# Kernel optimization log

Hardware: AMD Instinct MI355X
Metric: run time of the kernel (lower is better)

Reference implementation:

```python
import jax, jax.numpy as jnp
import numpy as np

B, S, D, H, KD, FF = 512, 128, 128, 8, 128, 512  # molecules, max atoms, embed, heads, key_dim(=embed), ffn
NEG = -1e9
EPS = 1e-3  # keras LayerNormalization default epsilon


def _layernorm(x, g, b):
    m = jnp.mean(x, axis=-1, keepdims=True)
    v = jnp.var(x, axis=-1, keepdims=True)
    return (x - m) * jax.lax.rsqrt(v + EPS) * g + b


def setup_inputs() -> dict:
    key = jax.random.key(0)
    k = jax.random.split(key, 8)
    # ragged molecule sizes in [32, 128]; deterministic so shapes are reproducible
    counts = 32 + ((np.arange(B) * 37) % 97)
    N = int(counts.sum())  # 40914
    mol = jnp.asarray(np.repeat(np.arange(B), counts), jnp.int32)  # sorted molecule ids
    picked = jnp.asarray((np.arange(B) * 13) % counts, jnp.int64)  # valid in-molecule atom index
    s = 0.05
    return {
        "atom_features": jax.random.normal(k[0], (N, D), jnp.float32),
        "Wq": jax.random.normal(k[1], (D, H, KD), jnp.float32) * s,
        "bq": jnp.zeros((H, KD), jnp.float32),
        "Wk": jax.random.normal(k[2], (D, H, KD), jnp.float32) * s,
        "bk": jnp.zeros((H, KD), jnp.float32),
        "Wv": jax.random.normal(k[3], (D, H, KD), jnp.float32) * s,
        "bv": jnp.zeros((H, KD), jnp.float32),
        "Wo": jax.random.normal(k[4], (H, KD, D), jnp.float32) * s,
        "bo": jnp.zeros((D,), jnp.float32),
        "W1": jax.random.normal(k[5], (D, FF), jnp.float32) * s,
        "b1": jnp.zeros((FF,), jnp.float32),
        "W2": jax.random.normal(k[6], (FF, D), jnp.float32) * s,
        "b2": jnp.zeros((D,), jnp.float32),
        "g1": jnp.ones((D,), jnp.float32),
        "beta1": jnp.zeros((D,), jnp.float32),
        "g2": jnp.ones((D,), jnp.float32),
        "beta2": jnp.zeros((D,), jnp.float32),
        "molecule_indicator": mol,
        "picked_atoms": picked,
    }


def _forward(atom_features, Wq, bq, Wk, bk, Wv, bv, Wo, bo, W1, b1, W2, b2,
             g1, beta1, g2, beta2, mol, picked):
    N = mol.shape[0]
    # --- PartitionPadding: pack ragged atoms -> [B, S, D] (every molecule nonempty,
    # so the zero-row filter keeps all B molecules in order) ---
    counts = jax.ops.segment_sum(jnp.ones((N,), jnp.int32), mol, num_segments=B)
    offsets = jnp.concatenate([jnp.zeros((1,), jnp.int32), jnp.cumsum(counts)[:-1]])
    pos = jnp.arange(N, dtype=jnp.int32) - offsets[mol]  # index within molecule
    x = jnp.zeros((B, S, D), atom_features.dtype).at[mol, pos].set(atom_features)
    mask = jnp.arange(S)[None, :] < counts[:, None]  # key padding mask [B, S]

    # --- masked MHA (keras MultiHeadAttention, key_dim = embed_dim) ---
    q = jnp.einsum('bsd,dhk->bshk', x, Wq) + bq
    kk = jnp.einsum('bsd,dhk->bshk', x, Wk) + bk
    v = jnp.einsum('bsd,dhk->bshk', x, Wv) + bv
    scores = jnp.einsum('bqhk,bshk->bhqs', q, kk) / jnp.sqrt(jnp.float32(KD))
    scores = jnp.where(mask[:, None, None, :], scores, NEG)
    attn = jax.nn.softmax(scores, axis=-1)
    ctx = jnp.einsum('bhqs,bshk->bqhk', attn, v)
    attn_out = jnp.einsum('bqhk,hkd->bqd', ctx, Wo) + bo

    # --- residual + LN + FFN + LN ---
    h = _layernorm(x + attn_out, g1, beta1)
    ffn = jax.nn.relu(h @ W1 + b1) @ W2 + b2
    out = _layernorm(h + ffn, g2, beta2)

    # --- gather_nd readout: one picked atom per molecule ---
    return out[jnp.arange(B), picked]  # [B, D]


def reference(atom_features, Wq, bq, Wk, bk, Wv, bv, Wo, bo, W1, b1, W2, b2,
              g1, beta1, g2, beta2, molecule_indicator, picked_atoms):
    return _forward(atom_features, Wq, bq, Wk, bk, Wv, bv, Wo, bo, W1, b1, W2, b2,
                    g1, beta1, g2, beta2, molecule_indicator, picked_atoms)
```

## Files before the change

kernel.cpp:

```cpp
#include <hip/hip_runtime.h>
#include <hip/hip_bf16.h>
#include <hip/hip_fp16.h>


#define BMOL 512

typedef _Float16 v2h __attribute__((ext_vector_type(2)));

#if defined(__has_builtin)
#if __has_builtin(__builtin_amdgcn_fdot2)
#define HAVE_FDOT2 1
#endif
#endif
static __device__ __forceinline__ float fdot2f(v2h a, v2h b, float c) {
#ifdef HAVE_FDOT2
    return __builtin_amdgcn_fdot2(a, b, c, false);
#else
    return c + (float)a[0] * (float)b[0] + (float)a[1] * (float)b[1];
#endif
}

__global__ __launch_bounds__(256) void k_front(
    const float* __restrict__ Wq, const float* __restrict__ bq,
    const float* __restrict__ Wk, const float* __restrict__ Wv,
    const float* __restrict__ Wo, const float* __restrict__ bv,
    const float* __restrict__ W1, const float* __restrict__ W2,
    const int* __restrict__ mol, int N, int noff,
    int* __restrict__ offs, __half* __restrict__ WVOp,
    __half* __restrict__ WQKp, float* __restrict__ bqk,
    float* __restrict__ bvoP, __half* __restrict__ W1p, __half* __restrict__ W2p)
{
    __shared__ float lds[2176];
    int bid = blockIdx.x, t = threadIdx.x;

    if (bid < 256) {
        bool qk = bid >= 128;
        int rel = bid & 127;
        int h = rel >> 4, tile = rel & 15;
        int dt = tile >> 2, ct = tile & 3;
        float* Avs = lds;
        float* Bos = lds + 1056;
        int ry = t >> 5, cx = t & 31;
        float acc[4] = {0.f, 0.f, 0.f, 0.f};
        const float* Asrc = qk ? Wq : Wv;
        for (int kk = 0; kk < 4; ++kk) {
            int r = t >> 3, e0 = (t & 7) * 4;
            float4 va = *(const float4*)(Asrc + (size_t)(dt * 32 + r) * 1024 + h * 128 + kk * 32 + e0);
            Avs[r * 33 + e0] = va.x; Avs[r * 33 + e0 + 1] = va.y;
            Avs[r * 33 + e0 + 2] = va.z; Avs[r * 33 + e0 + 3] = va.w;
            if (qk) {
                float4 vb = *(const float4*)(Wk + (size_t)(ct * 32 + r) * 1024 + h * 128 + kk * 32 + e0);
                Bos[(e0 + 0) * 33 + r] = vb.x;
                Bos[(e0 + 1) * 33 + r] = vb.y;
                Bos[(e0 + 2) * 33 + r] = vb.z;
                Bos[(e0 + 3) * 33 + r] = vb.w;
            } else {
                float4 vb = *(const float4*)(Wo + (size_t)h * 16384 + (size_t)(kk * 32 + r) * 128 + ct * 32 + e0);
                Bos[r * 33 + e0] = vb.x; Bos[r * 33 + e0 + 1] = vb.y;
                Bos[r * 33 + e0 + 2] = vb.z; Bos[r * 33 + e0 + 3] = vb.w;
            }
            __syncthreads();
            #pragma unroll
            for (int k = 0; k < 32; ++k) {
                float b = Bos[k * 33 + cx];
                #pragma unroll
                for (int i = 0; i < 4; ++i) acc[i] += Avs[(ry * 4 + i) * 33 + k] * b;
            }
            __syncthreads();
        }
        __half2 p0 = __floats2half2_rn(acc[0], acc[1]);
        __half2 p1 = __floats2half2_rn(acc[2], acc[3]);
        __half* dst = (qk ? WQKp : WVOp)
                    + (size_t)(h * 16 + dt * 4 + (ry >> 1)) * 1024
                    + (ct * 32 + cx) * 8 + (ry & 1) * 4;
        ((__half2*)dst)[0] = p0; ((__half2*)dst)[1] = p1;
        return;
    }
    bid -= 256;
    if (bid < 32) {
        int g = bid * 256 + t;
        int kg = g >> 9, f = g & 511;
        __half2 p[4];
        #pragma unroll
        for (int j = 0; j < 4; ++j) {
            float a = W1[(size_t)(kg * 8 + 2 * j) * 512 + f];
            float b = W1[(size_t)(kg * 8 + 2 * j + 1) * 512 + f];
            p[j] = __floats2half2_rn(a, b);
        }
        *(float4*)(W1p + (size_t)kg * 4096 + f * 8) = *(float4*)p;
        return;
    }
    bid -= 32;
    if (bid < 32) {
        int g = bid * 256 + t;
        int fg = g >> 7, c = g & 127;
        __half2 p[4];
        #pragma unroll
        for (int j = 0; j < 4; ++j) {
            float a = W2[(size_t)(fg * 8 + 2 * j) * 128 + c];
            float b = W2[(size_t)(fg * 8 + 2 * j + 1) * 128 + c];
            p[j] = __floats2half2_rn(a, b);
        }
        *(float4*)(W2p + (size_t)fg * 1024 + c * 8) = *(float4*)p;
        return;
    }
    bid -= 32;
    if (bid < 8) {
        int half = t >> 7, c = t & 127;
        float acc = 0.f;
        #pragma unroll 4
        for (int kk = 0; kk < 64; ++kk) {
            int k = bid * 128 + half * 64 + kk;
            acc += bv[k] * Wo[(size_t)k * 128 + c];
        }
        lds[half * 128 + c] = acc;
        __syncthreads();
        if (t < 128) bvoP[bid * 128 + t] = lds[t] + lds[128 + t];
        return;
    }
    bid -= 8;
    if (bid < 8) {
        int h = bid;
        if (t < 128) {
            const float* wk = Wk + (size_t)t * 1024 + h * 128;
            const float* bqh = bq + h * 128;
            float acc = 0.f;
            #pragma unroll 4
            for (int kd = 0; kd < 128; ++kd) acc += bqh[kd] * wk[kd];
            bqk[h * 128 + t] = acc;
        }
        return;
    }
    bid -= 8;
    {
        int i = bid * 256 + t;
        if (i < N) {
            if (i == 0) { offs[0] = 0; offs[BMOL] = N; }
            else if (mol[i] != mol[i - 1]) offs[mol[i]] = i;
        }
    }
}

__global__ __launch_bounds__(512) void k_attn_tail(
    const float* __restrict__ AF, const int* __restrict__ offs,
    const int* __restrict__ picked,
    const __half* __restrict__ WQKp, const float* __restrict__ bqk,
    const __half* __restrict__ WVOp, const float* __restrict__ bvoP,
    const float* __restrict__ bo,
    const float* __restrict__ g1, const float* __restrict__ be1,
    const __half* __restrict__ W1p, const float* __restrict__ b1,
    const __half* __restrict__ W2p, const float* __restrict__ b2,
    const float* __restrict__ g2, const float* __restrict__ be2,
    float* __restrict__ out)
{
    int b = blockIdx.x, t = threadIdx.x;
    int o0 = offs[b], cnt = offs[b + 1] - o0;
    __shared__ __half xs[128][136];
    __shared__ __half qsh[8][136];
    __shared__ float s[8 * 136];
    __shared__ float mh[8], lh[8];
    __shared__ float ws[2][1024];
    __shared__ __half wsh[1024];
    __shared__ float part[4][128];
    __shared__ float xp[128];
    __shared__ __half xph[128];
    __shared__ float h1raw[128], h1n[128];
    __shared__ __half h1nh[128];
    __shared__ __half msh[512];
    const float scale = 0.08838834764831843f;

    const float4* af4 = (const float4*)(AF + (size_t)o0 * 128);
    for (int p = t; p < cnt * 32; p += 512) {
        int i = p >> 5, d4 = p & 31;
        float4 v = af4[p];
        float2 st;
        ((__half2*)&st)[0] = __floats2half2_rn(v.x, v.y);
        ((__half2*)&st)[1] = __floats2half2_rn(v.z, v.w);
        *(float2*)(&xs[i][d4 * 4]) = st;
    }
    if (t < 128) {
        float v = AF[(size_t)(o0 + picked[b]) * 128 + t];
        xp[t] = v; xph[t] = (__half)v;
    }
    __syncthreads();
    {
        int h = t >> 6, d0 = (t & 63) * 2;
        const __half* wp = WQKp + ((size_t)(h * 16) * 128 + d0) * 8;
        const v2h* xh = (const v2h*)xph;
        float a0 = 0.f, a1 = 0.f;
        #pragma unroll 4
        for (int kg = 0; kg < 16; ++kg) {
            float4 r0 = *(const float4*)(wp + (size_t)kg * 1024);
            float4 r1 = *(const float4*)(wp + (size_t)kg * 1024 + 8);
            const v2h* h0 = (const v2h*)&r0;
            const v2h* h1 = (const v2h*)&r1;
            #pragma unroll
            for (int j = 0; j < 4; ++j) {
                v2h xv = xh[kg * 4 + j];
                a0 = fdot2f(xv, h0[j], a0);
                a1 = fdot2f(xv, h1[j], a1);
            }
        }
        qsh[h][d0]     = (__half)((a0 + bqk[h * 128 + d0]) * scale);
        qsh[h][d0 + 1] = (__half)((a1 + bqk[h * 128 + d0 + 1]) * scale);
    }
    __syncthreads();
    for (int p = t; p < cnt * 8; p += 512) {
        int i = p >> 3, h = p & 7;
        const float4* xr = (const float4*)xs[i];
        const float4* qr = (const float4*)qsh[h];
        float acc = 0.f;
        #pragma unroll 8
        for (int dq = 0; dq < 16; ++dq) {
            float4 xraw = xr[dq], qraw = qr[dq];
            const v2h* xh2 = (const v2h*)&xraw;
            const v2h* qh2 = (const v2h*)&qraw;
            acc = fdot2f(xh2[0], qh2[0], acc);
            acc = fdot2f(xh2[1], qh2[1], acc);
            acc = fdot2f(xh2[2], qh2[2], acc);
            acc = fdot2f(xh2[3], qh2[3], acc);
        }
        s[h * 136 + i] = acc;
    }
    __syncthreads();
    {
        int h = t >> 6, lane = t & 63;
        float m = -1e30f;
        for (int i = lane; i < cnt; i += 64) m = fmaxf(m, s[h * 136 + i]);
        #pragma unroll
        for (int off = 32; off; off >>= 1) m = fmaxf(m, __shfl_xor(m, off));
        float l = 0.f;
        for (int i = lane; i < cnt; i += 64) l += __expf(s[h * 136 + i] - m);
        #pragma unroll
        for (int off = 32; off; off >>= 1) l += __shfl_xor(l, off);
        if (lane == 0) { mh[h] = m; lh[h] = 1.f / l; }
    }
    __syncthreads();
    for (int p = t; p < cnt * 8; p += 512) {
        int i = p >> 3, h = p & 7;
        s[h * 136 + i] = __expf(s[h * 136 + i] - mh[h]) * lh[h];
    }
    __syncthreads();
    {
        int ih = t >> 8, hw = (t >> 5) & 7, qq = t & 31;
        float4 a4 = {0.f, 0.f, 0.f, 0.f};
        for (int i = ih; i < cnt; i += 2) {
            float sv = s[hw * 136 + i];
            float2 xraw = *(const float2*)(&xs[i][qq * 4]);
            const __half2* xh = (const __half2*)&xraw;
            float2 x0 = __half22float2(xh[0]), x1 = __half22float2(xh[1]);
            a4.x += sv * x0.x; a4.y += sv * x0.y; a4.z += sv * x1.x; a4.w += sv * x1.y;
        }
        *(float4*)(&ws[ih][hw * 128 + qq * 4]) = a4;
    }
    __syncthreads();
    {
        int k0 = t * 2;
        float v0 = ws[0][k0] + ws[1][k0];
        float v1 = ws[0][k0 + 1] + ws[1][k0 + 1];
        *(__half2*)(&wsh[k0]) = __floats2half2_rn(v0, v1);
    }
    __syncthreads();
    int wv = t >> 6, lane = t & 63;
    int kq = wv & 3, ch = wv >> 2;
    int c = ch * 64 + lane;
    {
        const __half* wp = WVOp + ((size_t)(kq * 32) * 128 + c) * 8;
        const v2h* wk = (const v2h*)wsh + kq * 128;
        float acc = 0.f;
        #pragma unroll 8
        for (int g = 0; g < 32; ++g) {
            float4 raw = *(const float4*)(wp + (size_t)g * 1024);
            const v2h* hp = (const v2h*)&raw;
            acc = fdot2f(hp[0], wk[g * 4 + 0], acc);
            acc = fdot2f(hp[1], wk[g * 4 + 1], acc);
            acc = fdot2f(hp[2], wk[g * 4 + 2], acc);
            acc = fdot2f(hp[3], wk[g * 4 + 3], acc);
        }
        part[kq][c] = acc;
    }
    __syncthreads();
    if (t < 128) {
        float acc = part[0][t] + part[1][t] + part[2][t] + part[3][t];
        float bias = bo[t];
        #pragma unroll
        for (int j = 0; j < 8; ++j) bias += bvoP[j * 128 + t];
        h1raw[t] = acc + bias + xp[t];
    }
    __syncthreads();
    {
        int l = t & 63;
        float a = h1raw[l], bb = h1raw[l + 64];
        float sm = a + bb, sq = a * a + bb * bb;
        #pragma unroll
        for (int off = 32; off; off >>= 1) { sm += __shfl_xor(sm, off); sq += __shfl_xor(sq, off); }
        float m = sm * (1.f / 128.f), var = sq * (1.f / 128.f) - m * m;
        float rs = rsqrtf(var + 1e-3f);
        if (t < 128) {
            float v = (h1raw[t] - m) * rs * g1[t] + be1[t];
            h1n[t] = v; h1nh[t] = (__half)v;
        }
    }
    __syncthreads();
    {
        const __half* wp = W1p + t * 8;
        const v2h* hk = (const v2h*)h1nh;
        float acc = 0.f;
        #pragma unroll 8
        for (int kg = 0; kg < 16; ++kg) {
            float4 raw = *(const float4*)(wp + (size_t)kg * 4096);
            const v2h* hp = (const v2h*)&raw;
            acc = fdot2f(hp[0], hk[kg * 4 + 0], acc);
            acc = fdot2f(hp[1], hk[kg * 4 + 1], acc);
            acc = fdot2f(hp[2], hk[kg * 4 + 2], acc);
            acc = fdot2f(hp[3], hk[kg * 4 + 3], acc);
        }
        msh[t] = (__half)fmaxf(acc + b1[t], 0.f);
    }
    __syncthreads();
    {
        const __half* wp = W2p + ((size_t)(kq * 16) * 128 + c) * 8;
        const v2h* mk = (const v2h*)msh + kq * 64;
        float acc = 0.f;
        #pragma unroll 8
        for (int g = 0; g < 16; ++g) {
            float4 raw = *(const float4*)(wp + (size_t)g * 1024);
            const v2h* hp = (const v2h*)&raw;
            acc = fdot2f(hp[0], mk[g * 4 + 0], acc);
            acc = fdot2f(hp[1], mk[g * 4 + 1], acc);
            acc = fdot2f(hp[2], mk[g * 4 + 2], acc);
            acc = fdot2f(hp[3], mk[g * 4 + 3], acc);
        }
        part[kq][c] = acc;
    }
    __syncthreads();
    if (t < 128) {
        float acc = part[0][t] + part[1][t] + part[2][t] + part[3][t];
        h1raw[t] = acc + b2[t] + h1n[t];
    }
    __syncthreads();
    {
        int l = t & 63;
        float a = h1raw[l], bb = h1raw[l + 64];
        float sm = a + bb, sq = a * a + bb * bb;
        #pragma unroll
        for (int off = 32; off; off >>= 1) { sm += __shfl_xor(sm, off); sq += __shfl_xor(sq, off); }
        float m = sm * (1.f / 128.f), var = sq * (1.f / 128.f) - m * m;
        float rs = rsqrtf(var + 1e-3f);
        if (t < 128) out[(size_t)b * 128 + t] = (h1raw[t] - m) * rs * g2[t] + be2[t];
    }
}

extern "C" void kernel_launch(void* const* d_in, const int* in_sizes, int n_in,
                              void* d_out, int out_size, void* d_ws, size_t ws_size,
                              hipStream_t stream) {
    const float* AF  = (const float*)d_in[0];
    const float* Wq  = (const float*)d_in[1];
    const float* bq  = (const float*)d_in[2];
    const float* Wk  = (const float*)d_in[3];
    const float* Wv  = (const float*)d_in[5];
    const float* bv  = (const float*)d_in[6];
    const float* Wo  = (const float*)d_in[7];
    const float* bo  = (const float*)d_in[8];
    const float* W1  = (const float*)d_in[9];
    const float* b1  = (const float*)d_in[10];
    const float* W2  = (const float*)d_in[11];
    const float* b2  = (const float*)d_in[12];
    const float* g1  = (const float*)d_in[13];
    const float* be1 = (const float*)d_in[14];
    const float* g2  = (const float*)d_in[15];
    const float* be2 = (const float*)d_in[16];
    const int* mol    = (const int*)d_in[17];
    const int* picked = (const int*)d_in[18];
    int N = in_sizes[0] / 128;
    int noff = (N + 255) / 256;

    char* ws = (char*)d_ws;
    int*    offs = (int*)ws;
    __half* WVOp = (__half*)(ws + 4096);
    __half* WQKp = (__half*)(ws + 266240);
    float*  bqk  = (float*)(ws + 528384);
    float*  bvoP = (float*)(ws + 532480);
    __half* W1p  = (__half*)(ws + 536576);
    __half* W2p  = (__half*)(ws + 667648);

    k_front<<<336 + noff, 256, 0, stream>>>(Wq, bq, Wk, Wv, Wo, bv, W1, W2,
                                            mol, N, noff,
                                            offs, WVOp, WQKp, bqk, bvoP, W1p, W2p);
    k_attn_tail<<<BMOL, 512, 0, stream>>>(AF, offs, picked, WQKp, bqk,
                                          WVOp, bvoP, bo, g1, be1, W1p, b1,
                                          W2p, b2, g2, be2, (float*)d_out);
}
```

Before: 36.05 us.

## Precompute per-molecule query projections in front kernel and batch tail over molecules

Query projection through Wq and Wk for each picked atom now runs in the front kernel: it binary-searches molecule offsets, loads picked rows and computes scaled query-key vectors per head, so the precomputed WQK product and bqk bias are no longer needed. The attention kernel only reads these vectors and writes the attention-weighted sums to workspace. A new tail kernel processes four molecules per block for Wo/V projection, layer norms and FFN, so each weight load is reused across four rows. This adds a third launch and a global round trip for intermediates, and puts more fp32 work in the front kernel.

```diff
diff --git a/kernel.cpp b/kernel.cpp
--- a/kernel.cpp
+++ b/kernel.cpp
@@ -21,44 +21,106 @@
 }
 
 __global__ __launch_bounds__(256) void k_front(
-    const float* __restrict__ Wq, const float* __restrict__ bq,
-    const float* __restrict__ Wk, const float* __restrict__ Wv,
-    const float* __restrict__ Wo, const float* __restrict__ bv,
-    const float* __restrict__ W1, const float* __restrict__ W2,
-    const int* __restrict__ mol, int N, int noff,
-    int* __restrict__ offs, __half* __restrict__ WVOp,
-    __half* __restrict__ WQKp, float* __restrict__ bqk,
-    float* __restrict__ bvoP, __half* __restrict__ W1p, __half* __restrict__ W2p)
+    const float* __restrict__ AF, const float* __restrict__ Wq,
+    const float* __restrict__ bq, const float* __restrict__ Wk,
+    const float* __restrict__ Wv, const float* __restrict__ Wo,
+    const float* __restrict__ bv, const float* __restrict__ W1,
+    const float* __restrict__ W2,
+    const int* __restrict__ mol, const int* __restrict__ picked,
+    int N, int noff,
+    int* __restrict__ offs, __half* __restrict__ QKh,
+    __half* __restrict__ WVOp, float* __restrict__ bvoP,
+    __half* __restrict__ W1p, __half* __restrict__ W2p)
 {
-    __shared__ float lds[2176];
+    __shared__ float smf[12672];
+    __shared__ int rows[16];
     int bid = blockIdx.x, t = threadIdx.x;
 
     if (bid < 256) {
-        bool qk = bid >= 128;
-        int rel = bid & 127;
-        int h = rel >> 4, tile = rel & 15;
+        int h = bid >> 5, m0 = (bid & 31) * 16;
+        float*  xp   = smf;
+        __half* wkTh = (__half*)(smf + 2048);
+        float*  q    = smf + 10496;
+        float*  bqks = smf + 12544;
+        const float scale = 0.08838834764831843f;
+        if (t < 16) {
+            int m = m0 + t;
+            int lo = 0, hi = N;
+            while (lo < hi) { int mid = (lo + hi) >> 1; if (mol[mid] < m) lo = mid + 1; else hi = mid; }
+            rows[t] = lo + picked[m];
+        }
+        {
+            int d = t & 127, kc = t >> 7;
+            #pragma unroll
+            for (int i = 0; i < 16; ++i) {
+                int kd0 = kc * 64 + i * 4;
+                float4 v = *(const float4*)(Wk + (size_t)d * 1024 + h * 128 + kd0);
+                wkTh[(kd0 + 0) * 132 + d] = (__half)v.x;
+                wkTh[(kd0 + 1) * 132 + d] = (__half)v.y;
+                wkTh[(kd0 + 2) * 132 + d] = (__half)v.z;
+                wkTh[(kd0 + 3) * 132 + d] = (__half)v.w;
+            }
+        }
+        __syncthreads();
+        for (int p = t; p < 512; p += 256) {
+            int m = p >> 5, d4 = p & 31;
+            ((float4*)(xp + m * 128))[d4] = ((const float4*)(AF + (size_t)rows[m] * 128))[d4];
+        }
+        if (t < 128) {
+            float acc = 0.f;
+            #pragma unroll 4
+            for (int k = 0; k < 128; ++k) acc += bq[h * 128 + k] * (float)wkTh[k * 132 + t];
+            bqks[t] = acc;
+        }
+        __syncthreads();
+        int c = t & 127, mg = t >> 7;
+        {
+            const float* wq = Wq + h * 128 + c;
+            float acc[8] = {0.f,0.f,0.f,0.f,0.f,0.f,0.f,0.f};
+            #pragma unroll 4
+            for (int k = 0; k < 128; ++k) {
+                float w = wq[(size_t)k * 1024];
+                const float* xk = xp + (mg * 8) * 128 + k;
+                #pragma unroll
+                for (int j = 0; j < 8; ++j) acc[j] += xk[j * 128] * w;
+            }
+            float bb = bq[h * 128 + c];
+            #pragma unroll
+            for (int j = 0; j < 8; ++j) q[(mg * 8 + j) * 128 + c] = acc[j] + bb;
+        }
+        __syncthreads();
+        {
+            float acc[8] = {0.f,0.f,0.f,0.f,0.f,0.f,0.f,0.f};
+            #pragma unroll 4
+            for (int k = 0; k < 128; ++k) {
+                float w = (float)wkTh[k * 132 + c];
+                const float* qk = q + (mg * 8) * 128 + k;
+                #pragma unroll
+                for (int j = 0; j < 8; ++j) acc[j] += qk[j * 128] * w;
+            }
+            float bb = bqks[c];
+            #pragma unroll
+            for (int j = 0; j < 8; ++j)
+                QKh[(size_t)(m0 + mg * 8 + j) * 1024 + h * 128 + c] = (__half)((acc[j] + bb) * scale);
+        }
+        return;
+    }
+    bid -= 256;
+    if (bid < 128) {
+        int h = bid >> 4, tile = bid & 15;
         int dt = tile >> 2, ct = tile & 3;
-        float* Avs = lds;
-        float* Bos = lds + 1056;
+        float* Avs = smf;
+        float* Bos = smf + 1056;
         int ry = t >> 5, cx = t & 31;
         float acc[4] = {0.f, 0.f, 0.f, 0.f};
-        const float* Asrc = qk ? Wq : Wv;
         for (int kk = 0; kk < 4; ++kk) {
             int r = t >> 3, e0 = (t & 7) * 4;
-            float4 va = *(const float4*)(Asrc + (size_t)(dt * 32 + r) * 1024 + h * 128 + kk * 32 + e0);
+            float4 va = *(const float4*)(Wv + (size_t)(dt * 32 + r) * 1024 + h * 128 + kk * 32 + e0);
             Avs[r * 33 + e0] = va.x; Avs[r * 33 + e0 + 1] = va.y;
             Avs[r * 33 + e0 + 2] = va.z; Avs[r * 33 + e0 + 3] = va.w;
-            if (qk) {
-                float4 vb = *(const float4*)(Wk + (size_t)(ct * 32 + r) * 1024 + h * 128 + kk * 32 + e0);
-                Bos[(e0 + 0) * 33 + r] = vb.x;
-                Bos[(e0 + 1) * 33 + r] = vb.y;
-                Bos[(e0 + 2) * 33 + r] = vb.z;
-                Bos[(e0 + 3) * 33 + r] = vb.w;
-            } else {
-                float4 vb = *(const float4*)(Wo + (size_t)h * 16384 + (size_t)(kk * 32 + r) * 128 + ct * 32 + e0);
-                Bos[r * 33 + e0] = vb.x; Bos[r * 33 + e0 + 1] = vb.y;
-                Bos[r * 33 + e0 + 2] = vb.z; Bos[r * 33 + e0 + 3] = vb.w;
-            }
+            float4 vb = *(const float4*)(Wo + (size_t)h * 16384 + (size_t)(kk * 32 + r) * 128 + ct * 32 + e0);
+            Bos[r * 33 + e0] = vb.x; Bos[r * 33 + e0 + 1] = vb.y;
+            Bos[r * 33 + e0 + 2] = vb.z; Bos[r * 33 + e0 + 3] = vb.w;
             __syncthreads();
             #pragma unroll
             for (int k = 0; k < 32; ++k) {
@@ -70,13 +132,12 @@
         }
         __half2 p0 = __floats2half2_rn(acc[0], acc[1]);
         __half2 p1 = __floats2half2_rn(acc[2], acc[3]);
-        __half* dst = (qk ? WQKp : WVOp)
-                    + (size_t)(h * 16 + dt * 4 + (ry >> 1)) * 1024
-                    + (ct * 32 + cx) * 8 + (ry & 1) * 4;
+        __half* dst = WVOp + (size_t)(h * 16 + dt * 4 + (ry >> 1)) * 1024
+                           + (ct * 32 + cx) * 8 + (ry & 1) * 4;
         ((__half2*)dst)[0] = p0; ((__half2*)dst)[1] = p1;
         return;
     }
-    bid -= 256;
+    bid -= 128;
     if (bid < 32) {
         int g = bid * 256 + t;
         int kg = g >> 9, f = g & 511;
@@ -113,22 +174,9 @@
             int k = bid * 128 + half * 64 + kk;
             acc += bv[k] * Wo[(size_t)k * 128 + c];
         }
-        lds[half * 128 + c] = acc;
+        smf[half * 128 + c] = acc;
         __syncthreads();
-        if (t < 128) bvoP[bid * 128 + t] = lds[t] + lds[128 + t];
-        return;
-    }
-    bid -= 8;
-    if (bid < 8) {
-        int h = bid;
-        if (t < 128) {
-            const float* wk = Wk + (size_t)t * 1024 + h * 128;
-            const float* bqh = bq + h * 128;
-            float acc = 0.f;
-            #pragma unroll 4
-            for (int kd = 0; kd < 128; ++kd) acc += bqh[kd] * wk[kd];
-            bqk[h * 128 + t] = acc;
-        }
+        if (t < 128) bvoP[bid * 128 + t] = smf[t] + smf[128 + t];
         return;
     }
     bid -= 8;
@@ -141,17 +189,9 @@
     }
 }
 
-__global__ __launch_bounds__(512) void k_attn_tail(
+__global__ __launch_bounds__(512) void k_attn(
     const float* __restrict__ AF, const int* __restrict__ offs,
-    const int* __restrict__ picked,
-    const __half* __restrict__ WQKp, const float* __restrict__ bqk,
-    const __half* __restrict__ WVOp, const float* __restrict__ bvoP,
-    const float* __restrict__ bo,
-    const float* __restrict__ g1, const float* __restrict__ be1,
-    const __half* __restrict__ W1p, const float* __restrict__ b1,
-    const __half* __restrict__ W2p, const float* __restrict__ b2,
-    const float* __restrict__ g2, const float* __restrict__ be2,
-    float* __restrict__ out)
+    const __half* __restrict__ QKh, __half* __restrict__ WXg)
 {
     int b = blockIdx.x, t = threadIdx.x;
     int o0 = offs[b], cnt = offs[b + 1] - o0;
@@ -160,14 +200,6 @@
     __shared__ float s[8 * 136];
     __shared__ float mh[8], lh[8];
     __shared__ float ws[2][1024];
-    __shared__ __half wsh[1024];
-    __shared__ float part[4][128];
-    __shared__ float xp[128];
-    __shared__ __half xph[128];
-    __shared__ float h1raw[128], h1n[128];
-    __shared__ __half h1nh[128];
-    __shared__ __half msh[512];
-    const float scale = 0.08838834764831843f;
 
     const float4* af4 = (const float4*)(AF + (size_t)o0 * 128);
     for (int p = t; p < cnt * 32; p += 512) {
@@ -179,30 +211,9 @@
         *(float2*)(&xs[i][d4 * 4]) = st;
     }
     if (t < 128) {
-        float v = AF[(size_t)(o0 + picked[b]) * 128 + t];
-        xp[t] = v; xph[t] = (__half)v;
-    }
-    __syncthreads();
-    {
-        int h = t >> 6, d0 = (t & 63) * 2;
-        const __half* wp = WQKp + ((size_t)(h * 16) * 128 + d0) * 8;
-        const v2h* xh = (const v2h*)xph;
-        float a0 = 0.f, a1 = 0.f;
-        #pragma unroll 4
-        for (int kg = 0; kg < 16; ++kg) {
-            float4 r0 = *(const float4*)(wp + (size_t)kg * 1024);
-            float4 r1 = *(const float4*)(wp + (size_t)kg * 1024 + 8);
-            const v2h* h0 = (const v2h*)&r0;
-            const v2h* h1 = (const v2h*)&r1;
-            #pragma unroll
-            for (int j = 0; j < 4; ++j) {
-                v2h xv = xh[kg * 4 + j];
-                a0 = fdot2f(xv, h0[j], a0);
-                a1 = fdot2f(xv, h1[j], a1);
-            }
-        }
-        qsh[h][d0]     = (__half)((a0 + bqk[h * 128 + d0]) * scale);
-        qsh[h][d0 + 1] = (__half)((a1 + bqk[h * 128 + d0 + 1]) * scale);
+        float4 ld = ((const float4*)(QKh + (size_t)b * 1024))[t];
+        int h = t >> 4, d0 = (t & 15) * 8;
+        *(float4*)(&qsh[h][d0]) = ld;
     }
     __syncthreads();
     for (int p = t; p < cnt * 8; p += 512) {
@@ -258,96 +269,122 @@
         int k0 = t * 2;
         float v0 = ws[0][k0] + ws[1][k0];
         float v1 = ws[0][k0 + 1] + ws[1][k0 + 1];
-        *(__half2*)(&wsh[k0]) = __floats2half2_rn(v0, v1);
-    }
-    __syncthreads();
-    int wv = t >> 6, lane = t & 63;
-    int kq = wv & 3, ch = wv >> 2;
-    int c = ch * 64 + lane;
-    {
-        const __half* wp = WVOp + ((size_t)(kq * 32) * 128 + c) * 8;
-        const v2h* wk = (const v2h*)wsh + kq * 128;
+        ((__half2*)(WXg + (size_t)b * 1024))[t] = __floats2half2_rn(v0, v1);
+    }
+}
+
+__global__ __launch_bounds__(512) void k_tail(
+    const float* __restrict__ AF, const int* __restrict__ offs,
+    const int* __restrict__ picked, const __half* __restrict__ WXg,
+    const __half* __restrict__ WVOp, const float* __restrict__ bvoP,
+    const float* __restrict__ bo,
+    const float* __restrict__ g1, const float* __restrict__ be1,
+    const __half* __restrict__ W1p, const float* __restrict__ b1,
+    const __half* __restrict__ W2p, const float* __restrict__ b2,
+    const float* __restrict__ g2, const float* __restrict__ be2,
+    float* __restrict__ out)
+{
+    int r0 = blockIdx.x * 4, t = threadIdx.x;
+    __shared__ __half wsh4[4][1024];
+    __shared__ float  xp4[4][128];
+    __shared__ float  h1raw[4][128];
+    __shared__ float  h1nf[4][128];
+    __shared__ __half h1nh[4][128];
+    __shared__ __half msh4[4][512];
+    __shared__ float  h2raw[4][128];
+    {
+        int rr = t >> 7, cc = t & 127;
+        ((float4*)(wsh4[rr]))[cc] = ((const float4*)(WXg + (size_t)(r0 + rr) * 1024))[cc];
+    }
+    if (t < 128) {
+        int rr = t >> 5, d4 = t & 31;
+        int row = offs[r0 + rr] + picked[r0 + rr];
+        ((float4*)(xp4[rr]))[d4] = ((const float4*)(AF + (size_t)row * 128))[d4];
+    }
+    __syncthreads();
+    int row = t >> 7, c = t & 127;
+    {
+        const __half* wp = WVOp + (size_t)c * 8;
+        const v2h* wk = (const v2h*)wsh4[row];
         float acc = 0.f;
         #pragma unroll 8
-        for (int g = 0; g < 32; ++g) {
-            float4 raw = *(const float4*)(wp + (size_t)g * 1024);
+        for (int kg = 0; kg < 128; ++kg) {
+            float4 raw = *(const float4*)(wp + (size_t)kg * 1024);
             const v2h* hp = (const v2h*)&raw;
-            acc = fdot2f(hp[0], wk[g * 4 + 0], acc);
-            acc = fdot2f(hp[1], wk[g * 4 + 1], acc);
-            acc = fdot2f(hp[2], wk[g * 4 + 2], acc);
-            acc = fdot2f(hp[3], wk[g * 4 + 3], acc);
-        }
-        part[kq][c] = acc;
-    }
-    __syncthreads();
-    if (t < 128) {
-        float acc = part[0][t] + part[1][t] + part[2][t] + part[3][t];
-        float bias = bo[t];
-        #pragma unroll
-        for (int j = 0; j < 8; ++j) bias += bvoP[j * 128 + t];
-        h1raw[t] = acc + bias + xp[t];
-    }
-    __syncthreads();
-    {
-        int l = t & 63;
-        float a = h1raw[l], bb = h1raw[l + 64];
-        float sm = a + bb, sq = a * a + bb * bb;
-        #pragma unroll
-        for (int off = 32; off; off >>= 1) { sm += __shfl_xor(sm, off); sq += __shfl_xor(sq, off); }
-        float m = sm * (1.f / 128.f), var = sq * (1.f / 128.f) - m * m;
-        float rs = rsqrtf(var + 1e-3f);
-        if (t < 128) {
-            float v = (h1raw[t] - m) * rs * g1[t] + be1[t];
-            h1n[t] = v; h1nh[t] = (__half)v;
+            acc = fdot2f(hp[0], wk[kg * 4 + 0], acc);
+            acc = fdot2f(hp[1], wk[kg * 4 + 1], acc);
+            acc = fdot2f(hp[2], wk[kg * 4 + 2], acc);
+            acc = fdot2f(hp[3], wk[kg * 4 + 3], acc);
+        }
+        float bias = bo[c];
+        #pragma unroll
+        for (int j = 0; j < 8; ++j) bias += bvoP[j * 128 + c];
+        h1raw[row][c] = acc + bias + xp4[row][c];
+    }
+    __syncthreads();
+    {
+        int wv = t >> 6, lane = t & 63;
+        if (wv < 4) {
+            float a = h1raw[wv][lane], bb = h1raw[wv][lane + 64];
+            float sm = a + bb, sq = a * a + bb * bb;
+            #pragma unroll
+            for (int off = 32; off; off >>= 1) { sm += __shfl_xor(sm, off); sq += __shfl_xor(sq, off); }
+            float m = sm * (1.f / 128.f), var = sq * (1.f / 128.f) - m * m;
+            float rs = rsqrtf(var + 1e-3f);
+            float va = (a - m) * rs * g1[lane] + be1[lane];
+            float vb = (bb - m) * rs * g1[lane + 64] + be1[lane + 64];
+            h1nf[wv][lane] = va;      h1nh[wv][lane] = (__half)va;
+            h1nf[wv][lane + 64] = vb; h1nh[wv][lane + 64] = (__half)vb;
         }
     }
     __syncthreads();
     {
         const __half* wp = W1p + t * 8;
-        const v2h* hk = (const v2h*)h1nh;
-        float acc = 0.f;
-        #pragma unroll 8
+        float acc[4] = {0.f, 0.f, 0.f, 0.f};
+        #pragma unroll 4
         for (int kg = 0; kg < 16; ++kg) {
             float4 raw = *(const float4*)(wp + (size_t)kg * 4096);
             const v2h* hp = (const v2h*)&raw;
-            acc = fdot2f(hp[0], hk[kg * 4 + 0], acc);
-            acc = fdot2f(hp[1], hk[kg * 4 + 1], acc);
-            acc = fdot2f(hp[2], hk[kg * 4 + 2], acc);
-            acc = fdot2f(hp[3], hk[kg * 4 + 3], acc);
-        }
-        msh[t] = (__half)fmaxf(acc + b1[t], 0.f);
-    }
-    __syncthreads();
-    {
-        const __half* wp = W2p + ((size_t)(kq * 16) * 128 + c) * 8;
-        const v2h* mk = (const v2h*)msh + kq * 64;
+            #pragma unroll
+            for (int j = 0; j < 4; ++j) {
+                #pragma unroll
+                for (int r = 0; r < 4; ++r)
+                    acc[r] = fdot2f(hp[j], ((const v2h*)h1nh[r])[kg * 4 + j], acc[r]);
+            }
+        }
+        float bb = b1[t];
+        #pragma unroll
+        for (int r = 0; r < 4; ++r) msh4[r][t] = (__half)fmaxf(acc[r] + bb, 0.f);
+    }
+    __syncthreads();
+    {
+        const __half* wp = W2p + (size_t)c * 8;
+        const v2h* mk = (const v2h*)msh4[row];
         float acc = 0.f;
         #pragma unroll 8
-        for (int g = 0; g < 16; ++g) {
-            float4 raw = *(const float4*)(wp + (size_t)g * 1024);
+        for (int kg = 0; kg < 64; ++kg) {
+            float4 raw = *(const float4*)(wp + (size_t)kg * 1024);
             const v2h* hp = (const v2h*)&raw;
-            acc = fdot2f(hp[0], mk[g * 4 + 0], acc);
-            acc = fdot2f(hp[1], mk[g * 4 + 1], acc);
-            acc = fdot2f(hp[2], mk[g * 4 + 2], acc);
-            acc = fdot2f(hp[3], mk[g * 4 + 3], acc);
-        }
-        part[kq][c] = acc;
-    }
-    __syncthreads();
-    if (t < 128) {
-        float acc = part[0][t] + part[1][t] + part[2][t] + part[3][t];
-        h1raw[t] = acc + b2[t] + h1n[t];
-    }
-    __syncthreads();
-    {
-        int l = t & 63;
-        float a = h1raw[l], bb = h1raw[l + 64];
-        float sm = a + bb, sq = a * a + bb * bb;
-        #pragma unroll
-        for (int off = 32; off; off >>= 1) { sm += __shfl_xor(sm, off); sq += __shfl_xor(sq, off); }
-        float m = sm * (1.f / 128.f), var = sq * (1.f / 128.f) - m * m;
-        float rs = rsqrtf(var + 1e-3f);
-        if (t < 128) out[(size_t)b * 128 + t] = (h1raw[t] - m) * rs * g2[t] + be2[t];
+            acc = fdot2f(hp[0], mk[kg * 4 + 0], acc);
+            acc = fdot2f(hp[1], mk[kg * 4 + 1], acc);
+            acc = fdot2f(hp[2], mk[kg * 4 + 2], acc);
+            acc = fdot2f(hp[3], mk[kg * 4 + 3], acc);
+        }
+        h2raw[row][c] = acc + b2[c] + h1nf[row][c];
+    }
+    __syncthreads();
+    {
+        int wv = t >> 6, lane = t & 63;
+        if (wv < 4) {
+            float a = h2raw[wv][lane], bb = h2raw[wv][lane + 64];
+            float sm = a + bb, sq = a * a + bb * bb;
+            #pragma unroll
+            for (int off = 32; off; off >>= 1) { sm += __shfl_xor(sm, off); sq += __shfl_xor(sq, off); }
+            float m = sm * (1.f / 128.f), var = sq * (1.f / 128.f) - m * m;
+            float rs = rsqrtf(var + 1e-3f);
+            out[(size_t)(r0 + wv) * 128 + lane]      = (a - m) * rs * g2[lane] + be2[lane];
+            out[(size_t)(r0 + wv) * 128 + lane + 64] = (bb - m) * rs * g2[lane + 64] + be2[lane + 64];
+        }
     }
 }
 
@@ -378,16 +415,17 @@
     char* ws = (char*)d_ws;
     int*    offs = (int*)ws;
     __half* WVOp = (__half*)(ws + 4096);
-    __half* WQKp = (__half*)(ws + 266240);
-    float*  bqk  = (float*)(ws + 528384);
-    float*  bvoP = (float*)(ws + 532480);
-    __half* W1p  = (__half*)(ws + 536576);
-    __half* W2p  = (__half*)(ws + 667648);
-
-    k_front<<<336 + noff, 256, 0, stream>>>(Wq, bq, Wk, Wv, Wo, bv, W1, W2,
-                                            mol, N, noff,
-                                            offs, WVOp, WQKp, bqk, bvoP, W1p, W2p);
-    k_attn_tail<<<BMOL, 512, 0, stream>>>(AF, offs, picked, WQKp, bqk,
-                                          WVOp, bvoP, bo, g1, be1, W1p, b1,
-                                          W2p, b2, g2, be2, (float*)d_out);
+    float*  bvoP = (float*)(ws + 266240);
+    __half* W1p  = (__half*)(ws + 270336);
+    __half* W2p  = (__half*)(ws + 401408);
+    __half* QKh  = (__half*)(ws + 532480);
+    __half* WXg  = (__half*)(ws + 1581056);
+
+    k_front<<<456 + noff, 256, 0, stream>>>(AF, Wq, bq, Wk, Wv, Wo, bv, W1, W2,
+                                            mol, picked, N, noff,
+                                            offs, QKh, WVOp, bvoP, W1p, W2p);
+    k_attn<<<BMOL, 512, 0, stream>>>(AF, offs, QKh, WXg);
+    k_tail<<<128, 512, 0, stream>>>(AF, offs, picked, WXg, WVOp, bvoP, bo,
+                                    g1, be1, W1p, b1, W2p, b2, g2, be2,
+                                    (float*)d_out);
 }
```

Result: slower. 61.47 us (+70.5%).

## Split attention and tail into two kernels, batching four molecules per tail block

Applied to the files above, without the earlier changes.

The fused attention+tail kernel is split. The attention kernel writes the per-molecule 1024-wide weighted-x vector to global memory as fp16. A new tail kernel then processes four molecules per block, so each WVO/W1/W2 weight load is reused across four rows. This aims to cut the weight traffic per molecule in the GEMV stages. In exchange it adds a kernel launch, a global round trip for the intermediate, and only 128 tail blocks. Each tail thread now runs the full K loop without a split-K reduction.

```diff
diff --git a/kernel.cpp b/kernel.cpp
--- a/kernel.cpp
+++ b/kernel.cpp
@@ -141,17 +141,11 @@
     }
 }
 
-__global__ __launch_bounds__(512) void k_attn_tail(
+__global__ __launch_bounds__(512) void k_attn(
     const float* __restrict__ AF, const int* __restrict__ offs,
     const int* __restrict__ picked,
     const __half* __restrict__ WQKp, const float* __restrict__ bqk,
-    const __half* __restrict__ WVOp, const float* __restrict__ bvoP,
-    const float* __restrict__ bo,
-    const float* __restrict__ g1, const float* __restrict__ be1,
-    const __half* __restrict__ W1p, const float* __restrict__ b1,
-    const __half* __restrict__ W2p, const float* __restrict__ b2,
-    const float* __restrict__ g2, const float* __restrict__ be2,
-    float* __restrict__ out)
+    __half* __restrict__ WXg)
 {
     int b = blockIdx.x, t = threadIdx.x;
     int o0 = offs[b], cnt = offs[b + 1] - o0;
@@ -160,13 +154,7 @@
     __shared__ float s[8 * 136];
     __shared__ float mh[8], lh[8];
     __shared__ float ws[2][1024];
-    __shared__ __half wsh[1024];
-    __shared__ float part[4][128];
-    __shared__ float xp[128];
     __shared__ __half xph[128];
-    __shared__ float h1raw[128], h1n[128];
-    __shared__ __half h1nh[128];
-    __shared__ __half msh[512];
     const float scale = 0.08838834764831843f;
 
     const float4* af4 = (const float4*)(AF + (size_t)o0 * 128);
@@ -178,10 +166,7 @@
         ((__half2*)&st)[1] = __floats2half2_rn(v.z, v.w);
         *(float2*)(&xs[i][d4 * 4]) = st;
     }
-    if (t < 128) {
-        float v = AF[(size_t)(o0 + picked[b]) * 128 + t];
-        xp[t] = v; xph[t] = (__half)v;
-    }
+    if (t < 128) xph[t] = (__half)AF[(size_t)(o0 + picked[b]) * 128 + t];
     __syncthreads();
     {
         int h = t >> 6, d0 = (t & 63) * 2;
@@ -258,96 +243,122 @@
         int k0 = t * 2;
         float v0 = ws[0][k0] + ws[1][k0];
         float v1 = ws[0][k0 + 1] + ws[1][k0 + 1];
-        *(__half2*)(&wsh[k0]) = __floats2half2_rn(v0, v1);
-    }
-    __syncthreads();
-    int wv = t >> 6, lane = t & 63;
-    int kq = wv & 3, ch = wv >> 2;
-    int c = ch * 64 + lane;
-    {
-        const __half* wp = WVOp + ((size_t)(kq * 32) * 128 + c) * 8;
-        const v2h* wk = (const v2h*)wsh + kq * 128;
+        ((__half2*)(WXg + (size_t)b * 1024))[t] = __floats2half2_rn(v0, v1);
+    }
+}
+
+__global__ __launch_bounds__(512) void k_tail(
+    const float* __restrict__ AF, const int* __restrict__ offs,
+    const int* __restrict__ picked, const __half* __restrict__ WXg,
+    const __half* __restrict__ WVOp, const float* __restrict__ bvoP,
+    const float* __restrict__ bo,
+    const float* __restrict__ g1, const float* __restrict__ be1,
+    const __half* __restrict__ W1p, const float* __restrict__ b1,
+    const __half* __restrict__ W2p, const float* __restrict__ b2,
+    const float* __restrict__ g2, const float* __restrict__ be2,
+    float* __restrict__ out)
+{
+    int r0 = blockIdx.x * 4, t = threadIdx.x;
+    __shared__ __half wsh4[4][1024];
+    __shared__ float  xp4[4][128];
+    __shared__ float  h1raw[4][128];
+    __shared__ float  h1nf[4][128];
+    __shared__ __half h1nh[4][128];
+    __shared__ __half msh4[4][512];
+    __shared__ float  h2raw[4][128];
+    {
+        int rr = t >> 7, cc = t & 127;
+        ((float4*)(wsh4[rr]))[cc] = ((const float4*)(WXg + (size_t)(r0 + rr) * 1024))[cc];
+    }
+    if (t < 128) {
+        int rr = t >> 5, d4 = t & 31;
+        int row = offs[r0 + rr] + picked[r0 + rr];
+        ((float4*)(xp4[rr]))[d4] = ((const float4*)(AF + (size_t)row * 128))[d4];
+    }
+    __syncthreads();
+    int row = t >> 7, c = t & 127;
+    {
+        const __half* wp = WVOp + (size_t)c * 8;
+        const v2h* wk = (const v2h*)wsh4[row];
         float acc = 0.f;
         #pragma unroll 8
-        for (int g = 0; g < 32; ++g) {
-            float4 raw = *(const float4*)(wp + (size_t)g * 1024);
+        for (int kg = 0; kg < 128; ++kg) {
+            float4 raw = *(const float4*)(wp + (size_t)kg * 1024);
             const v2h* hp = (const v2h*)&raw;
-            acc = fdot2f(hp[0], wk[g * 4 + 0], acc);
-            acc = fdot2f(hp[1], wk[g * 4 + 1], acc);
-            acc = fdot2f(hp[2], wk[g * 4 + 2], acc);
-            acc = fdot2f(hp[3], wk[g * 4 + 3], acc);
-        }
-        part[kq][c] = acc;
-    }
-    __syncthreads();
-    if (t < 128) {
-        float acc = part[0][t] + part[1][t] + part[2][t] + part[3][t];
-        float bias = bo[t];
-        #pragma unroll
-        for (int j = 0; j < 8; ++j) bias += bvoP[j * 128 + t];
-        h1raw[t] = acc + bias + xp[t];
-    }
-    __syncthreads();
-    {
-        int l = t & 63;
-        float a = h1raw[l], bb = h1raw[l + 64];
-        float sm = a + bb, sq = a * a + bb * bb;
-        #pragma unroll
-        for (int off = 32; off; off >>= 1) { sm += __shfl_xor(sm, off); sq += __shfl_xor(sq, off); }
-        float m = sm * (1.f / 128.f), var = sq * (1.f / 128.f) - m * m;
-        float rs = rsqrtf(var + 1e-3f);
-        if (t < 128) {
-            float v = (h1raw[t] - m) * rs * g1[t] + be1[t];
-            h1n[t] = v; h1nh[t] = (__half)v;
+            acc = fdot2f(hp[0], wk[kg * 4 + 0], acc);
+            acc = fdot2f(hp[1], wk[kg * 4 + 1], acc);
+            acc = fdot2f(hp[2], wk[kg * 4 + 2], acc);
+            acc = fdot2f(hp[3], wk[kg * 4 + 3], acc);
+        }
+        float bias = bo[c];
+        #pragma unroll
+        for (int j = 0; j < 8; ++j) bias += bvoP[j * 128 + c];
+        h1raw[row][c] = acc + bias + xp4[row][c];
+    }
+    __syncthreads();
+    {
+        int wv = t >> 6, lane = t & 63;
+        if (wv < 4) {
+            float a = h1raw[wv][lane], bb = h1raw[wv][lane + 64];
+            float sm = a + bb, sq = a * a + bb * bb;
+            #pragma unroll
+            for (int off = 32; off; off >>= 1) { sm += __shfl_xor(sm, off); sq += __shfl_xor(sq, off); }
+            float m = sm * (1.f / 128.f), var = sq * (1.f / 128.f) - m * m;
+            float rs = rsqrtf(var + 1e-3f);
+            float va = (a - m) * rs * g1[lane] + be1[lane];
+            float vb = (bb - m) * rs * g1[lane + 64] + be1[lane + 64];
+            h1nf[wv][lane] = va;      h1nh[wv][lane] = (__half)va;
+            h1nf[wv][lane + 64] = vb; h1nh[wv][lane + 64] = (__half)vb;
         }
     }
     __syncthreads();
     {
         const __half* wp = W1p + t * 8;
-        const v2h* hk = (const v2h*)h1nh;
-        float acc = 0.f;
-        #pragma unroll 8
+        float acc[4] = {0.f, 0.f, 0.f, 0.f};
+        #pragma unroll 4
         for (int kg = 0; kg < 16; ++kg) {
             float4 raw = *(const float4*)(wp + (size_t)kg * 4096);
             const v2h* hp = (const v2h*)&raw;
-            acc = fdot2f(hp[0], hk[kg * 4 + 0], acc);
-            acc = fdot2f(hp[1], hk[kg * 4 + 1], acc);
-            acc = fdot2f(hp[2], hk[kg * 4 + 2], acc);
-            acc = fdot2f(hp[3], hk[kg * 4 + 3], acc);
-        }
-        msh[t] = (__half)fmaxf(acc + b1[t], 0.f);
-    }
-    __syncthreads();
-    {
-        const __half* wp = W2p + ((size_t)(kq * 16) * 128 + c) * 8;
-        const v2h* mk = (const v2h*)msh + kq * 64;
+            #pragma unroll
+            for (int j = 0; j < 4; ++j) {
+                #pragma unroll
+                for (int r = 0; r < 4; ++r)
+                    acc[r] = fdot2f(hp[j], ((const v2h*)h1nh[r])[kg * 4 + j], acc[r]);
+            }
+        }
+        float bb = b1[t];
+        #pragma unroll
+        for (int r = 0; r < 4; ++r) msh4[r][t] = (__half)fmaxf(acc[r] + bb, 0.f);
+    }
+    __syncthreads();
+    {
+        const __half* wp = W2p + (size_t)c * 8;
+        const v2h* mk = (const v2h*)msh4[row];
         float acc = 0.f;
         #pragma unroll 8
-        for (int g = 0; g < 16; ++g) {
-            float4 raw = *(const float4*)(wp + (size_t)g * 1024);
+        for (int kg = 0; kg < 64; ++kg) {
+            float4 raw = *(const float4*)(wp + (size_t)kg * 1024);
             const v2h* hp = (const v2h*)&raw;
-            acc = fdot2f(hp[0], mk[g * 4 + 0], acc);
-            acc = fdot2f(hp[1], mk[g * 4 + 1], acc);
-            acc = fdot2f(hp[2], mk[g * 4 + 2], acc);
-            acc = fdot2f(hp[3], mk[g * 4 + 3], acc);
-        }
-        part[kq][c] = acc;
-    }
-    __syncthreads();
-    if (t < 128) {
-        float acc = part[0][t] + part[1][t] + part[2][t] + part[3][t];
-        h1raw[t] = acc + b2[t] + h1n[t];
-    }
-    __syncthreads();
-    {
-        int l = t & 63;
-        float a = h1raw[l], bb = h1raw[l + 64];
-        float sm = a + bb, sq = a * a + bb * bb;
-        #pragma unroll
-        for (int off = 32; off; off >>= 1) { sm += __shfl_xor(sm, off); sq += __shfl_xor(sq, off); }
-        float m = sm * (1.f / 128.f), var = sq * (1.f / 128.f) - m * m;
-        float rs = rsqrtf(var + 1e-3f);
-        if (t < 128) out[(size_t)b * 128 + t] = (h1raw[t] - m) * rs * g2[t] + be2[t];
+            acc = fdot2f(hp[0], mk[kg * 4 + 0], acc);
+            acc = fdot2f(hp[1], mk[kg * 4 + 1], acc);
+            acc = fdot2f(hp[2], mk[kg * 4 + 2], acc);
+            acc = fdot2f(hp[3], mk[kg * 4 + 3], acc);
+        }
+        h2raw[row][c] = acc + b2[c] + h1nf[row][c];
+    }
+    __syncthreads();
+    {
+        int wv = t >> 6, lane = t & 63;
+        if (wv < 4) {
+            float a = h2raw[wv][lane], bb = h2raw[wv][lane + 64];
+            float sm = a + bb, sq = a * a + bb * bb;
+            #pragma unroll
+            for (int off = 32; off; off >>= 1) { sm += __shfl_xor(sm, off); sq += __shfl_xor(sq, off); }
+            float m = sm * (1.f / 128.f), var = sq * (1.f / 128.f) - m * m;
+            float rs = rsqrtf(var + 1e-3f);
+            out[(size_t)(r0 + wv) * 128 + lane]      = (a - m) * rs * g2[lane] + be2[lane];
+            out[(size_t)(r0 + wv) * 128 + lane + 64] = (bb - m) * rs * g2[lane + 64] + be2[lane + 64];
+        }
     }
 }
 
@@ -383,11 +394,13 @@
     float*  bvoP = (float*)(ws + 532480);
     __half* W1p  = (__half*)(ws + 536576);
     __half* W2p  = (__half*)(ws + 667648);
+    __half* WXg  = (__half*)(ws + 798720);
 
     k_front<<<336 + noff, 256, 0, stream>>>(Wq, bq, Wk, Wv, Wo, bv, W1, W2,
                                             mol, N, noff,
                                             offs, WVOp, WQKp, bqk, bvoP, W1p, W2p);
-    k_attn_tail<<<BMOL, 512, 0, stream>>>(AF, offs, picked, WQKp, bqk,
-                                          WVOp, bvoP, bo, g1, be1, W1p, b1,
-                                          W2p, b2, g2, be2, (float*)d_out);
+    k_attn<<<BMOL, 512, 0, stream>>>(AF, offs, picked, WQKp, bqk, WXg);
+    k_tail<<<128, 512, 0, stream>>>(AF, offs, picked, WXg, WVOp, bvoP, bo,
+                                    g1, be1, W1p, b1, W2p, b2, g2, be2,
+                                    (float*)d_out);
 }
```

Result: slower. 45.20 us (+25.4%).

## Use MFMA 16x16x32 f16 for attention scores and probability-weighted sum

Applied to the files above, without the earlier changes.

Replaces the scalar fdot2 score computation and the FMA-based softmax-weighted accumulation with MFMA 16x16x32 f16 instructions. To fit the matrix tiles, the atom rows are zero-padded to a multiple of 32, the query and probability buffers are padded to 16 heads, and the probabilities are stored as f16. This removes the two-way partial-sum buffer and one synchronisation. In exchange it adds padding writes, a strided column gather from xs for the B operand, and f16 rounding of the attention probabilities.

```diff
diff --git a/kernel.cpp b/kernel.cpp
--- a/kernel.cpp
+++ b/kernel.cpp
@@ -6,6 +6,8 @@
 #define BMOL 512
 
 typedef _Float16 v2h __attribute__((ext_vector_type(2)));
+typedef _Float16 v8h __attribute__((ext_vector_type(8)));
+typedef float f32x4 __attribute__((ext_vector_type(4)));
 
 #if defined(__has_builtin)
 #if __has_builtin(__builtin_amdgcn_fdot2)
@@ -155,18 +157,19 @@
 {
     int b = blockIdx.x, t = threadIdx.x;
     int o0 = offs[b], cnt = offs[b + 1] - o0;
-    __shared__ __half xs[128][136];
-    __shared__ __half qsh[8][136];
+    int cpad = ((cnt + 31) >> 5) << 5;
+    __shared__ _Float16 xs[128][136];
+    __shared__ _Float16 qsh[16][136];
     __shared__ float s[8 * 136];
+    __shared__ _Float16 Ph[16][136];
     __shared__ float mh[8], lh[8];
-    __shared__ float ws[2][1024];
-    __shared__ __half wsh[1024];
+    __shared__ _Float16 wsh[1024];
     __shared__ float part[4][128];
     __shared__ float xp[128];
-    __shared__ __half xph[128];
+    __shared__ _Float16 xph[128];
     __shared__ float h1raw[128], h1n[128];
-    __shared__ __half h1nh[128];
-    __shared__ __half msh[512];
+    __shared__ _Float16 h1nh[128];
+    __shared__ _Float16 msh[512];
     const float scale = 0.08838834764831843f;
 
     const float4* af4 = (const float4*)(AF + (size_t)o0 * 128);
@@ -178,9 +181,18 @@
         ((__half2*)&st)[1] = __floats2half2_rn(v.z, v.w);
         *(float2*)(&xs[i][d4 * 4]) = st;
     }
+    for (int p = cnt * 32 + t; p < cpad * 32; p += 512) {
+        int i = p >> 5, d4 = p & 31;
+        float2 z = {0.f, 0.f};
+        *(float2*)(&xs[i][d4 * 4]) = z;
+    }
+    for (int p = t; p < 544; p += 512) {
+        ((unsigned*)&qsh[8][0])[p] = 0u;
+        ((unsigned*)&Ph[8][0])[p] = 0u;
+    }
     if (t < 128) {
         float v = AF[(size_t)(o0 + picked[b]) * 128 + t];
-        xp[t] = v; xph[t] = (__half)v;
+        xp[t] = v; xph[t] = (_Float16)v;
     }
     __syncthreads();
     {
@@ -201,26 +213,29 @@
                 a1 = fdot2f(xv, h1[j], a1);
             }
         }
-        qsh[h][d0]     = (__half)((a0 + bqk[h * 128 + d0]) * scale);
-        qsh[h][d0 + 1] = (__half)((a1 + bqk[h * 128 + d0 + 1]) * scale);
-    }
-    __syncthreads();
-    for (int p = t; p < cnt * 8; p += 512) {
-        int i = p >> 3, h = p & 7;
-        const float4* xr = (const float4*)xs[i];
-        const float4* qr = (const float4*)qsh[h];
-        float acc = 0.f;
-        #pragma unroll 8
-        for (int dq = 0; dq < 16; ++dq) {
-            float4 xraw = xr[dq], qraw = qr[dq];
-            const v2h* xh2 = (const v2h*)&xraw;
-            const v2h* qh2 = (const v2h*)&qraw;
-            acc = fdot2f(xh2[0], qh2[0], acc);
-            acc = fdot2f(xh2[1], qh2[1], acc);
-            acc = fdot2f(xh2[2], qh2[2], acc);
-            acc = fdot2f(xh2[3], qh2[3], acc);
-        }
-        s[h * 136 + i] = acc;
+        qsh[h][d0]     = (_Float16)((a0 + bqk[h * 128 + d0]) * scale);
+        qsh[h][d0 + 1] = (_Float16)((a1 + bqk[h * 128 + d0 + 1]) * scale);
+    }
+    __syncthreads();
+    {
+        int w = t >> 6, l = t & 63;
+        int i0 = w * 16;
+        if (i0 < cnt) {
+            int arow = i0 + (l & 15);
+            int q = l >> 4;
+            f32x4 acc = {0.f, 0.f, 0.f, 0.f};
+            #pragma unroll
+            for (int ks = 0; ks < 4; ++ks) {
+                v8h a  = *(const v8h*)(&xs[arow][ks * 32 + q * 8]);
+                v8h bf = *(const v8h*)(&qsh[l & 15][ks * 32 + q * 8]);
+                acc = __builtin_amdgcn_mfma_f32_16x16x32_f16(a, bf, acc, 0, 0, 0);
+            }
+            if ((l & 15) < 8) {
+                #pragma unroll
+                for (int r = 0; r < 4; ++r)
+                    s[(l & 15) * 136 + i0 + q * 4 + r] = acc[r];
+            }
+        }
     }
     __syncthreads();
     {
@@ -236,29 +251,31 @@
         if (lane == 0) { mh[h] = m; lh[h] = 1.f / l; }
     }
     __syncthreads();
-    for (int p = t; p < cnt * 8; p += 512) {
+    for (int p = t; p < cpad * 8; p += 512) {
         int i = p >> 3, h = p & 7;
-        s[h * 136 + i] = __expf(s[h * 136 + i] - mh[h]) * lh[h];
-    }
-    __syncthreads();
-    {
-        int ih = t >> 8, hw = (t >> 5) & 7, qq = t & 31;
-        float4 a4 = {0.f, 0.f, 0.f, 0.f};
-        for (int i = ih; i < cnt; i += 2) {
-            float sv = s[hw * 136 + i];
-            float2 xraw = *(const float2*)(&xs[i][qq * 4]);
-            const __half2* xh = (const __half2*)&xraw;
-            float2 x0 = __half22float2(xh[0]), x1 = __half22float2(xh[1]);
-            a4.x += sv * x0.x; a4.y += sv * x0.y; a4.z += sv * x1.x; a4.w += sv * x1.y;
-        }
-        *(float4*)(&ws[ih][hw * 128 + qq * 4]) = a4;
-    }
-    __syncthreads();
-    {
-        int k0 = t * 2;
-        float v0 = ws[0][k0] + ws[1][k0];
-        float v1 = ws[0][k0 + 1] + ws[1][k0 + 1];
-        *(__half2*)(&wsh[k0]) = __floats2half2_rn(v0, v1);
+        float v = (i < cnt) ? __expf(s[h * 136 + i] - mh[h]) * lh[h] : 0.f;
+        Ph[h][i] = (_Float16)v;
+    }
+    __syncthreads();
+    {
+        int w = t >> 6, l = t & 63;
+        int q = l >> 4;
+        int d0 = w * 16 + (l & 15);
+        int nks = cpad >> 5;
+        f32x4 acc = {0.f, 0.f, 0.f, 0.f};
+        for (int ks = 0; ks < nks; ++ks) {
+            int k0 = ks * 32 + q * 8;
+            v8h a = *(const v8h*)(&Ph[l & 15][k0]);
+            v8h bf;
+            #pragma unroll
+            for (int j = 0; j < 8; ++j) bf[j] = xs[k0 + j][d0];
+            acc = __builtin_amdgcn_mfma_f32_16x16x32_f16(a, bf, acc, 0, 0, 0);
+        }
+        #pragma unroll
+        for (int r = 0; r < 4; ++r) {
+            int h = q * 4 + r;
+            if (h < 8) wsh[h * 128 + d0] = (_Float16)acc[r];
+        }
     }
     __syncthreads();
     int wv = t >> 6, lane = t & 63;
@@ -298,7 +315,7 @@
         float rs = rsqrtf(var + 1e-3f);
         if (t < 128) {
             float v = (h1raw[t] - m) * rs * g1[t] + be1[t];
-            h1n[t] = v; h1nh[t] = (__half)v;
+            h1n[t] = v; h1nh[t] = (_Float16)v;
         }
     }
     __syncthreads();
@@ -315,7 +332,7 @@
             acc = fdot2f(hp[2], hk[kg * 4 + 2], acc);
             acc = fdot2f(hp[3], hk[kg * 4 + 3], acc);
         }
-        msh[t] = (__half)fmaxf(acc + b1[t], 0.f);
+        msh[t] = (_Float16)fmaxf(acc + b1[t], 0.f);
     }
     __syncthreads();
     {
```

New measurement: 32.52 us, median of 2. 9.8% less time.
